# Performance work log

Measured on AMD Instinct MI355X. Metric: run time of the kernel, lower is better.

## Reference

```python
import jax, jax.numpy as jnp
import numpy as np

HEADS = 8

def setup_inputs() -> dict:
    key = jax.random.key(0)
    ks = jax.random.split(key, 10)
    B, S, E = 2, 2048, 512
    q = jax.random.normal(ks[0], (B, S, E), jnp.float32)
    k = jax.random.normal(ks[1], (B, S, E), jnp.float32)
    v = jax.random.normal(ks[2], (B, S, E), jnp.float32)
    mask = jnp.zeros((S, S), jnp.float32)  # additive mask [s_q, s_k]
    scale = 0.02
    Wq = jax.random.normal(ks[3], (E, E), jnp.float32) * scale
    bq = jax.random.normal(ks[4], (E,), jnp.float32) * scale
    Wk = jax.random.normal(ks[5], (E, E), jnp.float32) * scale
    bk = jax.random.normal(ks[6], (E,), jnp.float32) * scale
    Wv = jax.random.normal(ks[7], (E, E), jnp.float32) * scale
    bv = jax.random.normal(ks[8], (E,), jnp.float32) * scale
    return {"q": q, "k": k, "v": v, "mask": mask,
            "Wq": Wq, "bq": bq, "Wk": Wk, "bk": bk, "Wv": Wv, "bv": bv}

def reference(q, k, v, mask, Wq, bq, Wk, bk, Wv, bv):
    H = HEADS
    b, s_q, _ = q.shape
    s_k = k.shape[1]
    s_v = v.shape[1]
    # NOTE: faithful to source: row-major view(b, H, s, -1) WITHOUT transposing
    # seq/head axes first (quirk of the original module).
    K = jnp.swapaxes((k @ Wk.T + bk).reshape(b, H, s_k, -1), 2, 3)  # [b,H,dh,s_k]
    Q = (q @ Wq.T + bq).reshape(b, H, s_q, -1)                      # [b,H,s_q,dh]
    V = (v @ Wv.T + bv).reshape(b, H, s_v, -1)                      # [b,H,s_v,dh]
    # NOTE: original scales by sqrt(K.shape[-1]) AFTER the transpose, i.e. sqrt(s_k)
    scores = (Q @ K) / jnp.sqrt(jnp.asarray(s_k, jnp.float32))      # [b,H,s_q,s_k]
    scores = scores + mask[:s_q, :s_k]
    attn = jax.nn.softmax(scores, axis=-1)
    out = (attn @ V).reshape(b, s_q, -1)  # [b, s_q, e]
    return out
```

## Files before the change

kernel.cpp:

```cpp
#include <hip/hip_runtime.h>


#define SEQ 2048
#define EMB 512
#define DH  64
#define MROWS 4096
#define NROWS 32768
#define L2E 1.4426950408889634f

typedef float  v4f __attribute__((ext_vector_type(4)));
typedef short  v8s __attribute__((ext_vector_type(8)));
typedef __fp16 v2h __attribute__((ext_vector_type(2)));

static __device__ __forceinline__ unsigned int f2bf(float f) {
    unsigned int u = __float_as_uint(f);
    u += 0x7fffu + ((u >> 16) & 1u);
    return u >> 16;
}
static __device__ __forceinline__ unsigned int pack2(float a, float b) {
    return f2bf(a) | (f2bf(b) << 16);
}
static __device__ __forceinline__ unsigned int cvtpk(float a, float b) {
    unsigned int r;
    asm("v_cvt_pk_bf16_f32 %0, %1, %2" : "=v"(r) : "v"(a), "v"(b));
    return r;
}
static __device__ __forceinline__ unsigned int packh2(float a, float b) {
    v2h h = __builtin_amdgcn_cvt_pkrtz(a, b);
    return __builtin_bit_cast(unsigned int, h);
}

__global__ __launch_bounds__(256, 3) void proj_kernel(
    const float* __restrict__ q, const float* __restrict__ k, const float* __restrict__ v,
    const float* __restrict__ Wq, const float* __restrict__ bq,
    const float* __restrict__ Wk, const float* __restrict__ bk,
    const float* __restrict__ Wv, const float* __restrict__ bv,
    const float* __restrict__ mask,
    unsigned short* __restrict__ Qbf, unsigned short* __restrict__ Kfr,
    unsigned short* __restrict__ Vbf, float* __restrict__ maskT,
    unsigned int* __restrict__ flagw)
{
    __shared__ __align__(16) char smem[27648];
    const int tid = threadIdx.x;

    if (blockIdx.x >= 768) {
        const int mb2 = blockIdx.x - 768;
        const int rb = mb2 >> 5, kt = mb2 & 31;
        float* tile = maskT + ((size_t)rb * 32 + kt) * 8192;
        float4 vals[8];
        bool any = false;
#pragma unroll
        for (int i = 0; i < 8; ++i) {
            int s = tid + i * 256;
            int l  = s & 63;
            int cb = (s >> 6) & 3;
            int g  = (s >> 8) & 1;
            int w2 = (s >> 9) & 3;
            int qd2 = l >> 4, n2 = l & 15;
            vals[i] = *(const float4*)&mask[
                (size_t)(rb * 128 + w2 * 32 + g * 16 + n2) * SEQ + kt * 64 + cb * 16 + qd2 * 4];
            any = any | (vals[i].x != 0.f) | (vals[i].y != 0.f)
                      | (vals[i].z != 0.f) | (vals[i].w != 0.f);
        }
        unsigned int* nzp = (unsigned int*)smem;
        if (tid == 0) *nzp = 0u;
        __syncthreads();
        if (any) *nzp = 1u;
        __syncthreads();
        if (tid == 0) flagw[rb * 32 + kt] = *nzp;
        if (*nzp) {
#pragma unroll
            for (int i = 0; i < 8; ++i) {
                int s = tid + i * 256;
                vals[i].x *= L2E; vals[i].y *= L2E;
                vals[i].z *= L2E; vals[i].w *= L2E;
                *(float4*)&tile[(size_t)s * 4] = vals[i];
            }
        }
        return;
    }

    char* As = smem;
    char* Ws = smem + 9216;

    const int id  = blockIdx.x;
    const int pos = id & 31;
    const int nb  = pos >> 3;
    const int unit = (id >> 5) * 8 + (pos & 7);
    const int mb = unit & 63;
    const int z  = unit >> 6;

    const float* A    = (z == 0) ? q  : (z == 1) ? k  : v;
    const float* W    = (z == 0) ? Wq : (z == 1) ? Wk : Wv;
    const float* bias = (z == 0) ? bq : (z == 1) ? bk : bv;
    unsigned short* Cg = (z == 0) ? Qbf : Vbf;

    const int w    = tid >> 6;
    const int lane = tid & 63;
    const int qd   = lane >> 4;
    const int n    = lane & 15;
    const int m0 = mb * 64, n0 = nb * 128;

    float4 areg[4], wreg[8];
#pragma unroll
    for (int i = 0; i < 4; ++i) {
        int c = tid + i * 256;
        areg[i] = *(const float4*)&A[(size_t)(m0 + (c >> 4)) * EMB + (c & 15) * 4];
    }
#pragma unroll
    for (int i = 0; i < 8; ++i) {
        int c = tid + i * 256;
        wreg[i] = *(const float4*)&W[(size_t)(n0 + (c >> 4)) * EMB + (c & 15) * 4];
    }

    v4f acc[8];
#pragma unroll
    for (int cb = 0; cb < 8; ++cb) acc[cb] = (v4f)0.f;

#pragma unroll 1
    for (int kt = 0; kt < 8; ++kt) {
        __syncthreads();
#pragma unroll
        for (int i = 0; i < 4; ++i) {
            int c = tid + i * 256;
            uint2 pk = { cvtpk(areg[i].x, areg[i].y), cvtpk(areg[i].z, areg[i].w) };
            *(uint2*)&As[(c >> 4) * 144 + (c & 15) * 8] = pk;
        }
#pragma unroll
        for (int i = 0; i < 8; ++i) {
            int c = tid + i * 256;
            uint2 pk = { cvtpk(wreg[i].x, wreg[i].y), cvtpk(wreg[i].z, wreg[i].w) };
            *(uint2*)&Ws[(c >> 4) * 144 + (c & 15) * 8] = pk;
        }
        __syncthreads();

        if (kt + 1 < 8) {
#pragma unroll
            for (int i = 0; i < 4; ++i) {
                int c = tid + i * 256;
                areg[i] = *(const float4*)&A[(size_t)(m0 + (c >> 4)) * EMB + (kt+1) * 64 + (c & 15) * 4];
            }
#pragma unroll
            for (int i = 0; i < 8; ++i) {
                int c = tid + i * 256;
                wreg[i] = *(const float4*)&W[(size_t)(n0 + (c >> 4)) * EMB + (kt+1) * 64 + (c & 15) * 4];
            }
        }

#pragma unroll
        for (int ks = 0; ks < 2; ++ks) {
            v8s af = *(const v8s*)&As[(w * 16 + n) * 144 + ks * 64 + qd * 16];
#pragma unroll
            for (int cb = 0; cb < 8; ++cb) {
                v8s bfr = *(const v8s*)&Ws[(cb * 16 + n) * 144 + ks * 64 + qd * 16];
                acc[cb] = __builtin_amdgcn_mfma_f32_16x16x32_bf16(af, bfr, acc[cb], 0, 0, 0);
            }
        }
    }

    const float osc = (z == 0) ? 0.031879357905f : 1.0f;
    float bb[8];
#pragma unroll
    for (int cb = 0; cb < 8; ++cb) bb[cb] = bias[n0 + cb * 16 + n];
#pragma unroll
    for (int cb = 0; cb < 8; ++cb)
#pragma unroll
        for (int r = 0; r < 4; ++r) acc[cb][r] = (acc[cb][r] + bb[cb]) * osc;

    __syncthreads();
    short* Ct = (short*)smem;
#pragma unroll
    for (int cb = 0; cb < 8; ++cb)
#pragma unroll
        for (int r = 0; r < 2; ++r) {
            unsigned int pk = cvtpk(acc[cb][2*r], acc[cb][2*r+1]);
            Ct[(w * 16 + qd * 4 + 2*r)     * 136 + cb * 16 + n] = (short)(pk & 0xffffu);
            Ct[(w * 16 + qd * 4 + 2*r + 1) * 136 + cb * 16 + n] = (short)(pk >> 16);
        }
    __syncthreads();
    const int rr = tid >> 2, q4 = tid & 3;
    if (z == 1) {
        const int bh = m0 >> 8;
        const int mm = (m0 & 255) + rr;
        unsigned short* Kh = Kfr + (size_t)bh * 32 * 4096;
#pragma unroll
        for (int i = 0; i < 4; ++i) {
            uint4 t4 = *(const uint4*)&smem[rr * 272 + q4 * 64 + i * 16];
            int nn = n0 + q4 * 32 + i * 8;
            int s  = mm * 8 + (nn >> 6);
            int kt = s >> 6, sk = s & 63;
            int dd = nn & 63;
            int entry = ((dd >> 5) * 4 + (sk >> 4)) * 64 + ((dd & 31) >> 3) * 16 + (sk & 15);
            *(uint4*)&Kh[(size_t)kt * 4096 + entry * 8] = t4;
        }
    } else {
#pragma unroll
        for (int i = 0; i < 4; ++i) {
            uint4 t4 = *(const uint4*)&smem[rr * 272 + q4 * 64 + i * 16];
            *(uint4*)&Cg[(size_t)(m0 + rr) * EMB + n0 + q4 * 32 + i * 8] = t4;
        }
    }
}

__global__ __launch_bounds__(256) void frag_kernel(
    const unsigned short* __restrict__ Vbf, unsigned short* __restrict__ Vfr)
{
    __shared__ unsigned short T[64 * 136];
    const int bh = blockIdx.x, kt = blockIdx.y;
    const int tid = threadIdx.x;

    const unsigned short* Vh = Vbf + (size_t)bh * (SEQ * DH) + (size_t)kt * 64 * DH;
#pragma unroll
    for (int i = 0; i < 2; ++i) {
        int c = tid + i * 256;
        int s_l = c >> 3, ch = c & 7;
        uint4 t4 = *(const uint4*)&Vh[c * 8];
        const unsigned short* e = (const unsigned short*)&t4;
#pragma unroll
        for (int j = 0; j < 8; ++j)
            T[(ch * 8 + j) * 136 + s_l] = e[j];
    }
    __syncthreads();
    unsigned short* Vo = Vfr + ((size_t)bh * 32 + kt) * 4096;
#pragma unroll
    for (int i = 0; i < 2; ++i) {
        int idx = tid + i * 256;
        int f = idx >> 6, l = idx & 63;
        int ks = f >> 2, cb = f & 3, qd = l >> 4, n = l & 15;
        uint4 t4 = *(const uint4*)&T[(cb * 16 + n) * 136 + ks * 32 + qd * 8];
        *(uint4*)&Vo[idx * 8] = t4;
    }
}

template <int SPLITS>
__global__ __launch_bounds__(256, 6) void attn_kernel(
    const unsigned short* __restrict__ Qbf,
    const unsigned short* __restrict__ Kfr, const unsigned short* __restrict__ Vfr,
    const float* __restrict__ maskT, const float* __restrict__ maskf,
    const unsigned int* __restrict__ flagw,
    unsigned short* __restrict__ Opart, float* __restrict__ ml,
    float* __restrict__ out)
{
    __shared__ __align__(16) char smem[17408];
    const int tid  = threadIdx.x;
    const int w    = tid >> 6;
    const int lane = tid & 63;
    const int qd   = lane >> 4;
    const int n    = lane & 15;
    const int a_   = qd & 1;
    const bool diag = (a_ == (qd >> 1));

    const int id = blockIdx.x;
    const int bh = (id & 7) * 2 + ((id >> 3) & 1);
    const int unit = id >> 4;
    const int rb6 = unit & 31;
    const int kq = unit >> 5;
    const int KT0 = kq * (32 / SPLITS), KT1 = KT0 + 32 / SPLITS;

    const unsigned short* Qh  = Qbf + (size_t)bh * (SEQ * DH);
    const unsigned short* Kfh = Kfr + (size_t)bh * 32 * 4096;
    const unsigned short* Vfh = Vfr + (size_t)bh * 32 * 4096;
    const unsigned int* fwb = flagw + (rb6 >> 1) * 32;

    v8s qf[2];
    {
        const size_t qrow = (size_t)(rb6 * 64 + w * 16 + n);
#pragma unroll
        for (int ks = 0; ks < 2; ++ks)
            qf[ks] = *(const v8s*)&Qh[qrow * DH + ks * 32 + qd * 8];
    }

    float l_ = 0.f;
    v4f oacc[4];
#pragma unroll
    for (int cb = 0; cb < 4; ++cb) oacc[cb] = (v4f)0.f;

#pragma unroll 1
    for (int kt = KT0; kt < KT1; ++kt) {
        const unsigned short* Kt = Kfh + (size_t)kt * 4096;
        const unsigned short* Vt = Vfh + (size_t)kt * 4096;

        v4f sacc[4];
        float4 mk[4];
        if (SPLITS > 1) {
            if (fwb[kt] != 0u) {
                const float* tileF = maskT + ((size_t)(rb6 >> 1) * 32 + kt) * 8192;
                const int wg = (rb6 & 1) * 4 + w;
#pragma unroll
                for (int cb = 0; cb < 4; ++cb)
                    sacc[cb] = *(const v4f*)&tileF[
                        (size_t)((wg * 4 + cb) * 64 + qd * 16 + n) * 4];
            } else {
#pragma unroll
                for (int cb = 0; cb < 4; ++cb) sacc[cb] = (v4f)0.f;
            }
        } else {
            const size_t mrow = (size_t)(rb6 * 64 + w * 16 + n);
#pragma unroll
            for (int cb = 0; cb < 4; ++cb) {
                mk[cb] = *(const float4*)&maskf[mrow * SEQ + kt * 64 + cb * 16 + qd * 4];
                sacc[cb] = (v4f)0.f;
            }
        }

#pragma unroll
        for (int ks = 0; ks < 2; ++ks)
#pragma unroll
            for (int cb = 0; cb < 4; ++cb) {
                v8s kf = *(const v8s*)&Kt[((ks * 4 + cb) * 64 + lane) * 8];
                sacc[cb] = __builtin_amdgcn_mfma_f32_16x16x32_bf16(kf, qf[ks], sacc[cb], 0, 0, 0);
            }

        v8s pfr[2];
        {
            float rs = 0.f;
            unsigned int O_[4][2];
#pragma unroll
            for (int cb = 0; cb < 4; ++cb) {
                float s0 = sacc[cb][0], s1 = sacc[cb][1];
                float s2 = sacc[cb][2], s3 = sacc[cb][3];
                if (SPLITS == 1) {
                    s0 = fmaf(mk[cb].x, L2E, s0);
                    s1 = fmaf(mk[cb].y, L2E, s1);
                    s2 = fmaf(mk[cb].z, L2E, s2);
                    s3 = fmaf(mk[cb].w, L2E, s3);
                }
                float e0 = __builtin_amdgcn_exp2f(s0);
                float e1 = __builtin_amdgcn_exp2f(s1);
                float e2 = __builtin_amdgcn_exp2f(s2);
                float e3 = __builtin_amdgcn_exp2f(s3);
                rs += (e0 + e1) + (e2 + e3);
                O_[cb][0] = pack2(e0, e1);
                O_[cb][1] = pack2(e2, e3);
            }
            rs += __shfl_xor(rs, 16);
            rs += __shfl_xor(rs, 32);
            l_ += rs;
#pragma unroll
            for (int ks = 0; ks < 2; ++ks) {
                unsigned int t0 = a_ ? O_[2 * ks][0] : O_[2 * ks + 1][0];
                unsigned int t1 = a_ ? O_[2 * ks][1] : O_[2 * ks + 1][1];
                unsigned int r0 = __shfl_xor(t0, 16);
                unsigned int r1 = __shfl_xor(t1, 16);
                unsigned int Z00 = a_ ? r0 : O_[2 * ks][0];
                unsigned int Z01 = a_ ? r1 : O_[2 * ks][1];
                unsigned int Z10 = a_ ? O_[2 * ks + 1][0] : r0;
                unsigned int Z11 = a_ ? O_[2 * ks + 1][1] : r1;
                unsigned int s00 = __shfl_xor(Z00, 48);
                unsigned int s01 = __shfl_xor(Z01, 48);
                unsigned int s10 = __shfl_xor(Z10, 48);
                unsigned int s11 = __shfl_xor(Z11, 48);
                uint4 pw;
                pw.x = diag ? Z00 : s00;
                pw.y = diag ? Z01 : s01;
                pw.z = diag ? Z10 : s10;
                pw.w = diag ? Z11 : s11;
                pfr[ks] = __builtin_bit_cast(v8s, pw);
            }
        }

#pragma unroll
        for (int ks = 0; ks < 2; ++ks)
#pragma unroll
            for (int cb = 0; cb < 4; ++cb) {
                v8s vf = *(const v8s*)&Vt[((ks * 4 + cb) * 64 + lane) * 8];
                oacc[cb] = __builtin_amdgcn_mfma_f32_16x16x32_bf16(vf, pfr[ks], oacc[cb], 0, 0, 0);
            }
    }

    if (SPLITS == 1) {
        const float inv = 1.0f / l_;
#pragma unroll
        for (int cb = 0; cb < 4; ++cb)
#pragma unroll
            for (int r = 0; r < 4; ++r) oacc[cb][r] *= inv;
    } else {
        if (qd == 0) {
            const size_t row = (size_t)bh * SEQ + rb6 * 64 + w * 16 + n;
            ml[(size_t)kq * NROWS + row] = l_;
        }
    }
    __syncthreads();
#pragma unroll
    for (int cb = 0; cb < 4; ++cb)
        *(v4f*)&smem[(w * 16 + n) * 272 + cb * 64 + qd * 16] = oacc[cb];
    __syncthreads();
    const int r_l = tid >> 2, q4 = tid & 3;
    if (SPLITS == 1) {
        float* dst = &out[((size_t)bh * SEQ + rb6 * 64 + r_l) * DH + q4 * 16];
#pragma unroll
        for (int i = 0; i < 4; ++i) {
            float4 t4 = *(const float4*)&smem[r_l * 272 + q4 * 64 + i * 16];
            *(float4*)&dst[i * 4] = t4;
        }
    } else {
        unsigned short* dst = &Opart[((size_t)kq * NROWS + (size_t)bh * SEQ + rb6 * 64 + r_l) * DH + q4 * 16];
#pragma unroll
        for (int i = 0; i < 2; ++i) {
            float4 f0 = *(const float4*)&smem[r_l * 272 + q4 * 64 + i * 32];
            float4 f1 = *(const float4*)&smem[r_l * 272 + q4 * 64 + i * 32 + 16];
            uint4 o = { packh2(f0.x, f0.y), packh2(f0.z, f0.w),
                        packh2(f1.x, f1.y), packh2(f1.z, f1.w) };
            *(uint4*)&dst[i * 8] = o;
        }
    }
}

__global__ __launch_bounds__(256) void combine_kernel(
    const unsigned int* __restrict__ Opart, const float* __restrict__ ml,
    float* __restrict__ out, int splits)
{
    const int tid = threadIdx.x;
    const size_t row = (size_t)blockIdx.x * 16 + (tid >> 4);
    const int d4 = (tid & 15) * 4;
    float denom = 0.f;
    float4 o = make_float4(0.f, 0.f, 0.f, 0.f);
    for (int s = 0; s < splits; ++s) {
        denom += ml[(size_t)s * NROWS + row];
        uint2 u = *(const uint2*)&Opart[((size_t)s * NROWS + row) * 32 + (d4 >> 1)];
        v2h h0 = __builtin_bit_cast(v2h, u.x);
        v2h h1 = __builtin_bit_cast(v2h, u.y);
        o.x += (float)h0.x; o.y += (float)h0.y;
        o.z += (float)h1.x; o.w += (float)h1.y;
    }
    const float inv = 1.0f / denom;
    o.x *= inv; o.y *= inv; o.z *= inv; o.w *= inv;
    *(float4*)&out[row * DH + d4] = o;
}

extern "C" void kernel_launch(void* const* d_in, const int* in_sizes, int n_in,
                              void* d_out, int out_size, void* d_ws, size_t ws_size,
                              hipStream_t stream) {
    const float* q    = (const float*)d_in[0];
    const float* k    = (const float*)d_in[1];
    const float* v    = (const float*)d_in[2];
    const float* mask = (const float*)d_in[3];
    const float* Wq   = (const float*)d_in[4];
    const float* bq   = (const float*)d_in[5];
    const float* Wk   = (const float*)d_in[6];
    const float* bk   = (const float*)d_in[7];
    const float* Wv   = (const float*)d_in[8];
    const float* bv   = (const float*)d_in[9];

    char* ws = (char*)d_ws;
    const size_t MB = 1024 * 1024;
    unsigned short* Qbf   = (unsigned short*)(ws + 0);
    unsigned short* Vfr   = (unsigned short*)(ws + 8 * MB);
    unsigned short* Opart = (unsigned short*)(ws + 12 * MB);
    unsigned short* Vbf   = (unsigned short*)(ws + 12 * MB);
    float*          mlp   = (float*)(ws + 28 * MB);
    unsigned int*   flagw = (unsigned int*)(ws + 28 * MB + 512 * 1024);
    float*          maskT = (float*)(ws + 29 * MB);

    const size_t need_split = 49 * MB;
    const bool do_split = ws_size >= need_split;

    if (do_split) {
        unsigned short* Kfr = (unsigned short*)(ws + 45 * MB);
        proj_kernel<<<1280, 256, 0, stream>>>(q, k, v, Wq, bq, Wk, bk, Wv, bv,
                                              mask, Qbf, Kfr, Vbf, maskT, flagw);
        dim3 tgrid(16, 32);
        frag_kernel<<<tgrid, 256, 0, stream>>>(Vbf, Vfr);
        attn_kernel<4><<<2048, 256, 0, stream>>>(Qbf, Kfr, Vfr, maskT, mask, flagw,
                                                 Opart, mlp, (float*)d_out);
        combine_kernel<<<NROWS / 16, 256, 0, stream>>>((const unsigned int*)Opart,
                                                       mlp, (float*)d_out, 4);
    } else {
        unsigned short* Kfr = (unsigned short*)(ws + 16 * MB);
        proj_kernel<<<768, 256, 0, stream>>>(q, k, v, Wq, bq, Wk, bk, Wv, bv,
                                             mask, Qbf, Kfr, Vbf, maskT, flagw);
        dim3 tgrid(16, 32);
        frag_kernel<<<tgrid, 256, 0, stream>>>(Vbf, Vfr);
        attn_kernel<1><<<512, 256, 0, stream>>>(Qbf, Kfr, Vfr, maskT, mask, flagw,
                                                Opart, mlp, (float*)d_out);
    }
}
```

Measured before the change: 167.4 us.

## Fuse projection, fragment, attention and combine into one cooperative persistent kernel

Turns the four kernels into device functions and runs them from a single cooperative kernel of 1024 blocks, with grid.sync between stages and each block looping over several virtual block ids. This is meant to remove the launch gaps and tail drain between the separate kernels. The price is that every stage runs with one shared launch config (the smem size of the largest stage, a fixed occupancy bound) and grid-wide barriers. If the cooperative launch fails, the old multi-kernel path is used instead.

```diff
diff --git a/kernel.cpp b/kernel.cpp
--- a/kernel.cpp
+++ b/kernel.cpp
@@ -1,4 +1,7 @@
 #include <hip/hip_runtime.h>
+#include <hip/hip_cooperative_groups.h>
+
+namespace cg = cooperative_groups;
 
 
 #define SEQ 2048
@@ -30,7 +33,7 @@
     return __builtin_bit_cast(unsigned int, h);
 }
 
-__global__ __launch_bounds__(256, 3) void proj_kernel(
+static __device__ void proj_body(int vb, char* smem,
     const float* __restrict__ q, const float* __restrict__ k, const float* __restrict__ v,
     const float* __restrict__ Wq, const float* __restrict__ bq,
     const float* __restrict__ Wk, const float* __restrict__ bk,
@@ -40,11 +43,10 @@
     unsigned short* __restrict__ Vbf, float* __restrict__ maskT,
     unsigned int* __restrict__ flagw)
 {
-    __shared__ __align__(16) char smem[27648];
     const int tid = threadIdx.x;
 
-    if (blockIdx.x >= 768) {
-        const int mb2 = blockIdx.x - 768;
+    if (vb >= 768) {
+        const int mb2 = vb - 768;
         const int rb = mb2 >> 5, kt = mb2 & 31;
         float* tile = maskT + ((size_t)rb * 32 + kt) * 8192;
         float4 vals[8];
@@ -83,7 +85,7 @@
     char* As = smem;
     char* Ws = smem + 9216;
 
-    const int id  = blockIdx.x;
+    const int id  = vb;
     const int pos = id & 31;
     const int nb  = pos >> 3;
     const int unit = (id >> 5) * 8 + (pos & 7);
@@ -202,11 +204,11 @@
     }
 }
 
-__global__ __launch_bounds__(256) void frag_kernel(
+static __device__ void frag_body(int vb, char* smemc,
     const unsigned short* __restrict__ Vbf, unsigned short* __restrict__ Vfr)
 {
-    __shared__ unsigned short T[64 * 136];
-    const int bh = blockIdx.x, kt = blockIdx.y;
+    unsigned short* T = (unsigned short*)smemc;
+    const int bh = vb & 15, kt = vb >> 4;
     const int tid = threadIdx.x;
 
     const unsigned short* Vh = Vbf + (size_t)bh * (SEQ * DH) + (size_t)kt * 64 * DH;
@@ -233,7 +235,7 @@
 }
 
 template <int SPLITS>
-__global__ __launch_bounds__(256, 6) void attn_kernel(
+static __device__ void attn_body(int id, char* smem,
     const unsigned short* __restrict__ Qbf,
     const unsigned short* __restrict__ Kfr, const unsigned short* __restrict__ Vfr,
     const float* __restrict__ maskT, const float* __restrict__ maskf,
@@ -241,7 +243,6 @@
     unsigned short* __restrict__ Opart, float* __restrict__ ml,
     float* __restrict__ out)
 {
-    __shared__ __align__(16) char smem[17408];
     const int tid  = threadIdx.x;
     const int w    = tid >> 6;
     const int lane = tid & 63;
@@ -250,7 +251,6 @@
     const int a_   = qd & 1;
     const bool diag = (a_ == (qd >> 1));
 
-    const int id = blockIdx.x;
     const int bh = (id & 7) * 2 + ((id >> 3) & 1);
     const int unit = id >> 4;
     const int rb6 = unit & 31;
@@ -406,18 +406,19 @@
     }
 }
 
-__global__ __launch_bounds__(256) void combine_kernel(
-    const unsigned int* __restrict__ Opart, const float* __restrict__ ml,
-    float* __restrict__ out, int splits)
+static __device__ void combine_body(int vb,
+    const unsigned short* __restrict__ Opart, const float* __restrict__ ml,
+    float* __restrict__ out)
 {
     const int tid = threadIdx.x;
-    const size_t row = (size_t)blockIdx.x * 16 + (tid >> 4);
+    const size_t row = (size_t)vb * 16 + (tid >> 4);
     const int d4 = (tid & 15) * 4;
     float denom = 0.f;
     float4 o = make_float4(0.f, 0.f, 0.f, 0.f);
-    for (int s = 0; s < splits; ++s) {
+#pragma unroll 1
+    for (int s = 0; s < 4; ++s) {
         denom += ml[(size_t)s * NROWS + row];
-        uint2 u = *(const uint2*)&Opart[((size_t)s * NROWS + row) * 32 + (d4 >> 1)];
+        uint2 u = *(const uint2*)&Opart[((size_t)s * NROWS + row) * DH + d4];
         v2h h0 = __builtin_bit_cast(v2h, u.x);
         v2h h1 = __builtin_bit_cast(v2h, u.y);
         o.x += (float)h0.x; o.y += (float)h0.y;
@@ -426,6 +427,79 @@
     const float inv = 1.0f / denom;
     o.x *= inv; o.y *= inv; o.z *= inv; o.w *= inv;
     *(float4*)&out[row * DH + d4] = o;
+}
+
+template <int SPLITS>
+__global__ __launch_bounds__(256, 4) void mega_kernel(
+    const float* q, const float* k, const float* v,
+    const float* Wq, const float* bq, const float* Wk, const float* bk,
+    const float* Wv, const float* bv, const float* mask,
+    unsigned short* Qbf, unsigned short* Kfr, unsigned short* Vbf,
+    unsigned short* Vfr, float* maskT, unsigned int* flagw,
+    unsigned short* Opart, float* ml, float* out)
+{
+    __shared__ __align__(16) char smem[27648];
+    cg::grid_group grid = cg::this_grid();
+    const int rb = blockIdx.x;
+
+    proj_body(rb, smem, q, k, v, Wq, bq, Wk, bk, Wv, bv, mask,
+              Qbf, Kfr, Vbf, maskT, flagw);
+    if (rb < 256) {
+        __syncthreads();
+        proj_body(rb + 1024, smem, q, k, v, Wq, bq, Wk, bk, Wv, bv, mask,
+                  Qbf, Kfr, Vbf, maskT, flagw);
+    }
+    grid.sync();
+
+    if (rb < 512) frag_body(rb, smem, Vbf, Vfr);
+    grid.sync();
+
+    if (SPLITS == 4) {
+        attn_body<4>(rb, smem, Qbf, Kfr, Vfr, maskT, mask, flagw, Opart, ml, out);
+        attn_body<4>(rb + 1024, smem, Qbf, Kfr, Vfr, maskT, mask, flagw, Opart, ml, out);
+        grid.sync();
+        combine_body(rb,        Opart, ml, out);
+        combine_body(rb + 1024, Opart, ml, out);
+    } else {
+        if (rb < 512)
+            attn_body<1>(rb, smem, Qbf, Kfr, Vfr, maskT, mask, flagw, Opart, ml, out);
+    }
+}
+
+__global__ __launch_bounds__(256, 3) void proj_kernel(
+    const float* q, const float* k, const float* v,
+    const float* Wq, const float* bq, const float* Wk, const float* bk,
+    const float* Wv, const float* bv, const float* mask,
+    unsigned short* Qbf, unsigned short* Kfr, unsigned short* Vbf,
+    float* maskT, unsigned int* flagw)
+{
+    __shared__ __align__(16) char smem[27648];
+    proj_body(blockIdx.x, smem, q, k, v, Wq, bq, Wk, bk, Wv, bv, mask,
+              Qbf, Kfr, Vbf, maskT, flagw);
+}
+
+__global__ __launch_bounds__(256) void frag_kernel(
+    const unsigned short* Vbf, unsigned short* Vfr)
+{
+    __shared__ __align__(16) char smem[17408];
+    frag_body(blockIdx.y * 16 + blockIdx.x, smem, Vbf, Vfr);
+}
+
+template <int SPLITS>
+__global__ __launch_bounds__(256, 6) void attn_kernel(
+    const unsigned short* Qbf, const unsigned short* Kfr, const unsigned short* Vfr,
+    const float* maskT, const float* maskf, const unsigned int* flagw,
+    unsigned short* Opart, float* ml, float* out)
+{
+    __shared__ __align__(16) char smem[17408];
+    attn_body<SPLITS>(blockIdx.x, smem, Qbf, Kfr, Vfr, maskT, maskf, flagw,
+                      Opart, ml, out);
+}
+
+__global__ __launch_bounds__(256) void combine_kernel(
+    const unsigned short* Opart, const float* ml, float* out)
+{
+    combine_body(blockIdx.x, Opart, ml, out);
 }
 
 extern "C" void kernel_launch(void* const* d_in, const int* in_sizes, int n_in,
@@ -455,23 +529,39 @@
     const size_t need_split = 49 * MB;
     const bool do_split = ws_size >= need_split;
 
+    unsigned short* Kfr = do_split ? (unsigned short*)(ws + 45 * MB)
+                                   : (unsigned short*)(ws + 16 * MB);
+    float* outp = (float*)d_out;
+
+    {
+        void* args[] = { (void*)&q, (void*)&k, (void*)&v,
+                         (void*)&Wq, (void*)&bq, (void*)&Wk, (void*)&bk,
+                         (void*)&Wv, (void*)&bv, (void*)&mask,
+                         (void*)&Qbf, (void*)&Kfr, (void*)&Vbf, (void*)&Vfr,
+                         (void*)&maskT, (void*)&flagw,
+                         (void*)&Opart, (void*)&mlp, (void*)&outp };
+        void* fn = do_split ? reinterpret_cast<void*>(&mega_kernel<4>)
+                            : reinterpret_cast<void*>(&mega_kernel<1>);
+        hipError_t err = hipLaunchCooperativeKernel(fn, dim3(1024), dim3(256),
+                                                    args, 0, stream);
+        if (err == hipSuccess) return;
+        (void)hipGetLastError();
+    }
+
     if (do_split) {
-        unsigned short* Kfr = (unsigned short*)(ws + 45 * MB);
         proj_kernel<<<1280, 256, 0, stream>>>(q, k, v, Wq, bq, Wk, bk, Wv, bv,
                                               mask, Qbf, Kfr, Vbf, maskT, flagw);
         dim3 tgrid(16, 32);
         frag_kernel<<<tgrid, 256, 0, stream>>>(Vbf, Vfr);
         attn_kernel<4><<<2048, 256, 0, stream>>>(Qbf, Kfr, Vfr, maskT, mask, flagw,
-                                                 Opart, mlp, (float*)d_out);
-        combine_kernel<<<NROWS / 16, 256, 0, stream>>>((const unsigned int*)Opart,
-                                                       mlp, (float*)d_out, 4);
+                                                 Opart, mlp, outp);
+        combine_kernel<<<NROWS / 16, 256, 0, stream>>>(Opart, mlp, outp);
     } else {
-        unsigned short* Kfr = (unsigned short*)(ws + 16 * MB);
         proj_kernel<<<768, 256, 0, stream>>>(q, k, v, Wq, bq, Wk, bk, Wv, bv,
                                              mask, Qbf, Kfr, Vbf, maskT, flagw);
         dim3 tgrid(16, 32);
         frag_kernel<<<tgrid, 256, 0, stream>>>(Vbf, Vfr);
         attn_kernel<1><<<512, 256, 0, stream>>>(Qbf, Kfr, Vfr, maskT, mask, flagw,
-                                                Opart, mlp, (float*)d_out);
-    }
-}
+                                                Opart, mlp, outp);
+    }
+}
```

New measurement: 616.7 us. 269% more time.

## Software-pipeline K fragment loads with register double buffering in attention loop

Applied to the files above, without the earlier changes.

Unrolls the key-tile loop by two and prefetches the next tile's K fragments into a second register buffer while the current tile is computed, so global load latency overlaps the MFMA and softmax work. Launch bounds drop from 6 to 4 waves per SIMD to make room for the extra registers. This trades occupancy for instruction-level overlap, and it assumes the number of key tiles per split is even.

```diff
diff --git a/kernel.cpp b/kernel.cpp
--- a/kernel.cpp
+++ b/kernel.cpp
@@ -232,8 +232,103 @@
     }
 }
 
+
+#define ATTN_STEP(KT, KC, KN, DOPF)                                            \
+    {                                                                           \
+        if (DOPF) {                                                             \
+            const unsigned short* Kn = Kfh + (size_t)((KT) + 1) * 4096;         \
+            _Pragma("unroll")                                                   \
+            for (int f = 0; f < 8; ++f)                                         \
+                KN[f] = *(const v8s*)&Kn[(f * 64 + lane) * 8];                  \
+        }                                                                       \
+        const unsigned short* Vt = Vfh + (size_t)(KT) * 4096;                   \
+        v4f sacc[4];                                                            \
+        float4 mk[4];                                                           \
+        if (SPLITS > 1) {                                                       \
+            if (fwb[(KT)] != 0u) {                                              \
+                const float* tileF = maskT + ((size_t)(rb6 >> 1) * 32 + (KT)) * 8192; \
+                const int wg = (rb6 & 1) * 4 + w;                               \
+                _Pragma("unroll")                                               \
+                for (int cb = 0; cb < 4; ++cb)                                  \
+                    sacc[cb] = *(const v4f*)&tileF[                             \
+                        (size_t)((wg * 4 + cb) * 64 + qd * 16 + n) * 4];        \
+            } else {                                                            \
+                _Pragma("unroll")                                               \
+                for (int cb = 0; cb < 4; ++cb) sacc[cb] = (v4f)0.f;             \
+            }                                                                   \
+        } else {                                                                \
+            const size_t mrow = (size_t)(rb6 * 64 + w * 16 + n);                \
+            _Pragma("unroll")                                                   \
+            for (int cb = 0; cb < 4; ++cb) {                                    \
+                mk[cb] = *(const float4*)&maskf[mrow * SEQ + (KT) * 64 + cb * 16 + qd * 4]; \
+                sacc[cb] = (v4f)0.f;                                            \
+            }                                                                   \
+        }                                                                       \
+        _Pragma("unroll")                                                       \
+        for (int ks = 0; ks < 2; ++ks)                                          \
+            _Pragma("unroll")                                                   \
+            for (int cb = 0; cb < 4; ++cb)                                      \
+                sacc[cb] = __builtin_amdgcn_mfma_f32_16x16x32_bf16(             \
+                    KC[ks * 4 + cb], qf[ks], sacc[cb], 0, 0, 0);                \
+        v8s pfr[2];                                                             \
+        {                                                                       \
+            float rs = 0.f;                                                     \
+            unsigned int O_[4][2];                                              \
+            _Pragma("unroll")                                                   \
+            for (int cb = 0; cb < 4; ++cb) {                                    \
+                float s0 = sacc[cb][0], s1 = sacc[cb][1];                       \
+                float s2 = sacc[cb][2], s3 = sacc[cb][3];                       \
+                if (SPLITS == 1) {                                              \
+                    s0 = fmaf(mk[cb].x, L2E, s0);                               \
+                    s1 = fmaf(mk[cb].y, L2E, s1);                               \
+                    s2 = fmaf(mk[cb].z, L2E, s2);                               \
+                    s3 = fmaf(mk[cb].w, L2E, s3);                               \
+                }                                                               \
+                float e0 = __builtin_amdgcn_exp2f(s0);                          \
+                float e1 = __builtin_amdgcn_exp2f(s1);                          \
+                float e2 = __builtin_amdgcn_exp2f(s2);                          \
+                float e3 = __builtin_amdgcn_exp2f(s3);                          \
+                rs += (e0 + e1) + (e2 + e3);                                    \
+                O_[cb][0] = pack2(e0, e1);                                      \
+                O_[cb][1] = pack2(e2, e3);                                      \
+            }                                                                   \
+            rs += __shfl_xor(rs, 16);                                           \
+            rs += __shfl_xor(rs, 32);                                           \
+            l_ += rs;                                                           \
+            _Pragma("unroll")                                                   \
+            for (int ks = 0; ks < 2; ++ks) {                                    \
+                unsigned int t0 = a_ ? O_[2 * ks][0] : O_[2 * ks + 1][0];       \
+                unsigned int t1 = a_ ? O_[2 * ks][1] : O_[2 * ks + 1][1];       \
+                unsigned int r0 = __shfl_xor(t0, 16);                           \
+                unsigned int r1 = __shfl_xor(t1, 16);                           \
+                unsigned int Z00 = a_ ? r0 : O_[2 * ks][0];                     \
+                unsigned int Z01 = a_ ? r1 : O_[2 * ks][1];                     \
+                unsigned int Z10 = a_ ? O_[2 * ks + 1][0] : r0;                 \
+                unsigned int Z11 = a_ ? O_[2 * ks + 1][1] : r1;                 \
+                unsigned int s00 = __shfl_xor(Z00, 48);                         \
+                unsigned int s01 = __shfl_xor(Z01, 48);                         \
+                unsigned int s10 = __shfl_xor(Z10, 48);                         \
+                unsigned int s11 = __shfl_xor(Z11, 48);                         \
+                uint4 pw;                                                       \
+                pw.x = diag ? Z00 : s00;                                        \
+                pw.y = diag ? Z01 : s01;                                        \
+                pw.z = diag ? Z10 : s10;                                        \
+                pw.w = diag ? Z11 : s11;                                        \
+                pfr[ks] = __builtin_bit_cast(v8s, pw);                          \
+            }                                                                   \
+        }                                                                       \
+        _Pragma("unroll")                                                       \
+        for (int ks = 0; ks < 2; ++ks)                                          \
+            _Pragma("unroll")                                                   \
+            for (int cb = 0; cb < 4; ++cb) {                                    \
+                v8s vf = *(const v8s*)&Vt[((ks * 4 + cb) * 64 + lane) * 8];     \
+                oacc[cb] = __builtin_amdgcn_mfma_f32_16x16x32_bf16(             \
+                    vf, pfr[ks], oacc[cb], 0, 0, 0);                            \
+            }                                                                   \
+    }
+
 template <int SPLITS>
-__global__ __launch_bounds__(256, 6) void attn_kernel(
+__global__ __launch_bounds__(256, 4) void attn_kernel(
     const unsigned short* __restrict__ Qbf,
     const unsigned short* __restrict__ Kfr, const unsigned short* __restrict__ Vfr,
     const float* __restrict__ maskT, const float* __restrict__ maskf,
@@ -275,97 +370,18 @@
 #pragma unroll
     for (int cb = 0; cb < 4; ++cb) oacc[cb] = (v4f)0.f;
 
+    v8s ka[8], kb[8];
+    {
+        const unsigned short* K0 = Kfh + (size_t)KT0 * 4096;
+#pragma unroll
+        for (int f = 0; f < 8; ++f)
+            ka[f] = *(const v8s*)&K0[(f * 64 + lane) * 8];
+    }
+
 #pragma unroll 1
-    for (int kt = KT0; kt < KT1; ++kt) {
-        const unsigned short* Kt = Kfh + (size_t)kt * 4096;
-        const unsigned short* Vt = Vfh + (size_t)kt * 4096;
-
-        v4f sacc[4];
-        float4 mk[4];
-        if (SPLITS > 1) {
-            if (fwb[kt] != 0u) {
-                const float* tileF = maskT + ((size_t)(rb6 >> 1) * 32 + kt) * 8192;
-                const int wg = (rb6 & 1) * 4 + w;
-#pragma unroll
-                for (int cb = 0; cb < 4; ++cb)
-                    sacc[cb] = *(const v4f*)&tileF[
-                        (size_t)((wg * 4 + cb) * 64 + qd * 16 + n) * 4];
-            } else {
-#pragma unroll
-                for (int cb = 0; cb < 4; ++cb) sacc[cb] = (v4f)0.f;
-            }
-        } else {
-            const size_t mrow = (size_t)(rb6 * 64 + w * 16 + n);
-#pragma unroll
-            for (int cb = 0; cb < 4; ++cb) {
-                mk[cb] = *(const float4*)&maskf[mrow * SEQ + kt * 64 + cb * 16 + qd * 4];
-                sacc[cb] = (v4f)0.f;
-            }
-        }
-
-#pragma unroll
-        for (int ks = 0; ks < 2; ++ks)
-#pragma unroll
-            for (int cb = 0; cb < 4; ++cb) {
-                v8s kf = *(const v8s*)&Kt[((ks * 4 + cb) * 64 + lane) * 8];
-                sacc[cb] = __builtin_amdgcn_mfma_f32_16x16x32_bf16(kf, qf[ks], sacc[cb], 0, 0, 0);
-            }
-
-        v8s pfr[2];
-        {
-            float rs = 0.f;
-            unsigned int O_[4][2];
-#pragma unroll
-            for (int cb = 0; cb < 4; ++cb) {
-                float s0 = sacc[cb][0], s1 = sacc[cb][1];
-                float s2 = sacc[cb][2], s3 = sacc[cb][3];
-                if (SPLITS == 1) {
-                    s0 = fmaf(mk[cb].x, L2E, s0);
-                    s1 = fmaf(mk[cb].y, L2E, s1);
-                    s2 = fmaf(mk[cb].z, L2E, s2);
-                    s3 = fmaf(mk[cb].w, L2E, s3);
-                }
-                float e0 = __builtin_amdgcn_exp2f(s0);
-                float e1 = __builtin_amdgcn_exp2f(s1);
-                float e2 = __builtin_amdgcn_exp2f(s2);
-                float e3 = __builtin_amdgcn_exp2f(s3);
-                rs += (e0 + e1) + (e2 + e3);
-                O_[cb][0] = pack2(e0, e1);
-                O_[cb][1] = pack2(e2, e3);
-            }
-            rs += __shfl_xor(rs, 16);
-            rs += __shfl_xor(rs, 32);
-            l_ += rs;
-#pragma unroll
-            for (int ks = 0; ks < 2; ++ks) {
-                unsigned int t0 = a_ ? O_[2 * ks][0] : O_[2 * ks + 1][0];
-                unsigned int t1 = a_ ? O_[2 * ks][1] : O_[2 * ks + 1][1];
-                unsigned int r0 = __shfl_xor(t0, 16);
-                unsigned int r1 = __shfl_xor(t1, 16);
-                unsigned int Z00 = a_ ? r0 : O_[2 * ks][0];
-                unsigned int Z01 = a_ ? r1 : O_[2 * ks][1];
-                unsigned int Z10 = a_ ? O_[2 * ks + 1][0] : r0;
-                unsigned int Z11 = a_ ? O_[2 * ks + 1][1] : r1;
-                unsigned int s00 = __shfl_xor(Z00, 48);
-                unsigned int s01 = __shfl_xor(Z01, 48);
-                unsigned int s10 = __shfl_xor(Z10, 48);
-                unsigned int s11 = __shfl_xor(Z11, 48);
-                uint4 pw;
-                pw.x = diag ? Z00 : s00;
-                pw.y = diag ? Z01 : s01;
-                pw.z = diag ? Z10 : s10;
-                pw.w = diag ? Z11 : s11;
-                pfr[ks] = __builtin_bit_cast(v8s, pw);
-            }
-        }
-
-#pragma unroll
-        for (int ks = 0; ks < 2; ++ks)
-#pragma unroll
-            for (int cb = 0; cb < 4; ++cb) {
-                v8s vf = *(const v8s*)&Vt[((ks * 4 + cb) * 64 + lane) * 8];
-                oacc[cb] = __builtin_amdgcn_mfma_f32_16x16x32_bf16(vf, pfr[ks], oacc[cb], 0, 0, 0);
-            }
+    for (int kt2 = KT0; kt2 < KT1; kt2 += 2) {
+        ATTN_STEP(kt2,     ka, kb, true);
+        ATTN_STEP(kt2 + 1, kb, ka, (kt2 + 2 < KT1));
     }
 
     if (SPLITS == 1) {
```

New measurement: 174.0 us. 4.0% more time.
